# Optimization experiments

Hardware: AMD Instinct MI355X
Metric: run time of the kernel (lower is better)

## Reference

```python
import jax, jax.numpy as jnp
import numpy as np

N_NODES = 100000
IN_DIM = 128
HIDDEN = 64
N_EDGES = 1600000


def setup_inputs() -> dict:
    key = jax.random.key(0)
    k_z, k_e, k_w1, k_b1, k_w2, k_b2 = jax.random.split(key, 6)
    z = jax.random.normal(k_z, (N_NODES, IN_DIM), dtype=jnp.float32)
    edge_index = jax.random.randint(k_e, (2, N_EDGES), 0, N_NODES, dtype=jnp.int64)
    # PyTorch Linear stores weight [out, in]; keep [in, out] layout for x @ W
    bound1 = 1.0 / np.sqrt(2 * IN_DIM)
    W1 = jax.random.uniform(k_w1, (2 * IN_DIM, HIDDEN), jnp.float32, -bound1, bound1)
    b1 = jax.random.uniform(k_b1, (HIDDEN,), jnp.float32, -bound1, bound1)
    bound2 = 1.0 / np.sqrt(HIDDEN)
    W2 = jax.random.uniform(k_w2, (HIDDEN, 1), jnp.float32, -bound2, bound2)
    b2 = jax.random.uniform(k_b2, (1,), jnp.float32, -bound2, bound2)
    return {"z": z, "edge_index": edge_index, "W1": W1, "b1": b1, "W2": W2, "b2": b2}


def reference(z, edge_index, W1, b1, W2, b2):
    src = edge_index[0]
    dst = edge_index[1]
    # gather node features and concat: [E, 2*D]
    edge_feat = jnp.concatenate([z[src], z[dst]], axis=-1)
    h = jax.nn.relu(edge_feat @ W1 + b1)  # [E, H]
    logits = h @ W2 + b2                  # [E, 1]
    return jax.nn.sigmoid(logits).squeeze(-1)  # [E]
```

## Files before the change

kernel.cpp:

```cpp
#include <hip/hip_runtime.h>
#include <hip/hip_bf16.h>

#define N_NODES 100000
#define IN_DIM  128
#define HIDDEN  64
#define N_EDGES 1600000

typedef unsigned short u16;
typedef unsigned int   u32;
typedef unsigned char  u8;

typedef __attribute__((ext_vector_type(8))) short bf16x8;
typedef __attribute__((ext_vector_type(4))) float f32x4;
typedef __attribute__((ext_vector_type(2))) float f32x2;

__device__ __forceinline__ u16 f2bf(float f) {
    u32 u = __float_as_uint(f);
    u32 r = 0x7FFFu + ((u >> 16) & 1u);
    u += r;
    return (u16)(u >> 16);
}

__device__ __forceinline__ u8 f2fp8(float f) {
    u32 p = (u32)__builtin_amdgcn_cvt_pk_fp8_f32(f, f, 0, false);
    return (u8)(p & 0xFF);
}

__global__ __launch_bounds__(256) void prep_kernel(const float* __restrict__ W1,
                                                   u16* __restrict__ WcatT) {
    int idx = blockIdx.x * 256 + threadIdx.x;
    int jj = idx >> 7;
    int k  = idx & 127;
    float v = (jj < 64) ? W1[k * 64 + jj] : W1[(128 + k) * 64 + (jj - 64)];
    WcatT[idx] = f2bf(v);
}

#define LDK 136
#define GEMM_BLOCKS 625

__global__ __launch_bounds__(256) void gemm_kernel(const float* __restrict__ z,
                                                   const u16* __restrict__ WcatT,
                                                   const float* __restrict__ b1,
                                                   u8* __restrict__ UVq) {
    __shared__ u16 Bs[128 * LDK];

    int tid = threadIdx.x;
    for (int c = tid; c < 128 * 16; c += 256) {
        int row = c >> 4, cc = c & 15;
        *(uint4*)(Bs + row * LDK + cc * 8) = *(const uint4*)(WcatT + row * 128 + cc * 8);
    }
    __syncthreads();

    int wave = tid >> 6;
    int lane = tid & 63;
    int quad = lane >> 4;
    int l16  = lane & 15;

    int gwid   = blockIdx.x * 4 + wave;
    int nwaves = GEMM_BLOCKS * 4;
    const int NTILES = N_NODES / 16;

    float bias[4];
#pragma unroll
    for (int nt = 0; nt < 4; nt++) bias[nt] = b1[nt * 16 + l16];

    for (int t = gwid; t < NTILES; t += nwaves) {
        const float* zrow = z + (size_t)(t * 16 + l16) * 128;

        float4 fa[8];
#pragma unroll
        for (int kb = 0; kb < 4; kb++) {
            fa[kb * 2]     = *(const float4*)(zrow + kb * 32 + quad * 8);
            fa[kb * 2 + 1] = *(const float4*)(zrow + kb * 32 + quad * 8 + 4);
        }
        bf16x8 afrag[4];
#pragma unroll
        for (int kb = 0; kb < 4; kb++) {
            union { bf16x8 v; u32 w[4]; } pk;
            float4 lo = fa[kb * 2], hi = fa[kb * 2 + 1];
            pk.w[0] = (u32)f2bf(lo.x) | ((u32)f2bf(lo.y) << 16);
            pk.w[1] = (u32)f2bf(lo.z) | ((u32)f2bf(lo.w) << 16);
            pk.w[2] = (u32)f2bf(hi.x) | ((u32)f2bf(hi.y) << 16);
            pk.w[3] = (u32)f2bf(hi.z) | ((u32)f2bf(hi.w) << 16);
            afrag[kb] = pk.v;
        }

        f32x4 acc[8];
        const f32x4 z4 = {0.f, 0.f, 0.f, 0.f};
#pragma unroll
        for (int i = 0; i < 8; i++) acc[i] = z4;

#pragma unroll
        for (int kb = 0; kb < 4; kb++) {
            int k0 = kb * 32 + quad * 8;
#pragma unroll
            for (int nt = 0; nt < 8; nt++) {
                bf16x8 b = *(const bf16x8*)(Bs + (nt * 16 + l16) * LDK + k0);
                acc[nt] = __builtin_amdgcn_mfma_f32_16x16x32_bf16(afrag[kb], b, acc[nt], 0, 0, 0);
            }
        }

#pragma unroll
        for (int nt = 0; nt < 8; nt++) {
            float bb = (nt < 4) ? bias[nt] : 0.f;
#pragma unroll
            for (int r = 0; r < 4; r++) {
                int row = t * 16 + quad * 4 + r;
                UVq[(size_t)row * 128 + nt * 16 + l16] = f2fp8(acc[nt][r] + bb);
            }
        }
    }
}

#define BATCH 8

__global__ __launch_bounds__(256, 2) void edge_kernel(const int* __restrict__ ei,
                                                      const u8* __restrict__ UVq,
                                                      const float* __restrict__ W2,
                                                      const float* __restrict__ b2,
                                                      float* __restrict__ out) {
    int gwave = (blockIdx.x * 256 + threadIdx.x) >> 6;
    int lane  = threadIdx.x & 63;
    int sub   = lane >> 3;
    int c     = lane & 7;

    float4 w2a = *(const float4*)(W2 + c * 8);
    float4 w2b = *(const float4*)(W2 + c * 8 + 4);
    float w2r[8] = {w2a.x, w2a.y, w2a.z, w2a.w, w2b.x, w2b.y, w2b.z, w2b.w};
    float b2v = b2[0];

    int ebase = gwave * 64 + sub;

    int sB[BATCH], dB[BATCH];
#pragma unroll
    for (int j = 0; j < BATCH; j++) {
        int e = ebase + j * 8;
        sB[j] = __builtin_nontemporal_load(ei + e);
        dB[j] = __builtin_nontemporal_load(ei + N_EDGES + e);
    }
    uint2 aB[BATCH], bB[BATCH];
#pragma unroll
    for (int j = 0; j < BATCH; j++) {
        aB[j] = *(const uint2*)(UVq + (size_t)sB[j] * 128 + c * 8);
        bB[j] = *(const uint2*)(UVq + (size_t)dB[j] * 128 + 64 + c * 8);
    }
    __builtin_amdgcn_sched_barrier(0);

#pragma unroll
    for (int j = 0; j < BATCH; j++) {
        u32 aw[2] = {aB[j].x, aB[j].y};
        u32 bw[2] = {bB[j].x, bB[j].y};
        float acc = 0.f;
#pragma unroll
        for (int i = 0; i < 2; i++) {
            f32x2 uu0 = __builtin_amdgcn_cvt_pk_f32_fp8(aw[i], false);
            f32x2 vv0 = __builtin_amdgcn_cvt_pk_f32_fp8(bw[i], false);
            f32x2 uu1 = __builtin_amdgcn_cvt_pk_f32_fp8(aw[i], true);
            f32x2 vv1 = __builtin_amdgcn_cvt_pk_f32_fp8(bw[i], true);
            float h0 = fmaxf(uu0.x + vv0.x, 0.f);
            float h1 = fmaxf(uu0.y + vv0.y, 0.f);
            float h2 = fmaxf(uu1.x + vv1.x, 0.f);
            float h3 = fmaxf(uu1.y + vv1.y, 0.f);
            acc = fmaf(h0, w2r[i * 4 + 0], acc);
            acc = fmaf(h1, w2r[i * 4 + 1], acc);
            acc = fmaf(h2, w2r[i * 4 + 2], acc);
            acc = fmaf(h3, w2r[i * 4 + 3], acc);
        }
        acc += __shfl_xor(acc, 1);
        acc += __shfl_xor(acc, 2);
        acc += __shfl_xor(acc, 4);
        if (c == 0) {
            float x = acc + b2v;
            __builtin_nontemporal_store(1.f / (1.f + __expf(-x)), out + ebase + j * 8);
        }
    }
}

extern "C" void kernel_launch(void* const* d_in, const int* in_sizes, int n_in,
                              void* d_out, int out_size, void* d_ws, size_t ws_size,
                              hipStream_t stream) {
    const float* z  = (const float*)d_in[0];
    const int*   ei = (const int*)d_in[1];
    const float* W1 = (const float*)d_in[2];
    const float* b1 = (const float*)d_in[3];
    const float* W2 = (const float*)d_in[4];
    const float* b2 = (const float*)d_in[5];
    float* out = (float*)d_out;

    u16* WcatT = (u16*)d_ws;
    u8*  UVq   = (u8*)((char*)d_ws + 65536);

    prep_kernel<<<64, 256, 0, stream>>>(W1, WcatT);
    gemm_kernel<<<GEMM_BLOCKS, 256, 0, stream>>>(z, WcatT, b1, UVq);
    edge_kernel<<<6250, 256, 0, stream>>>(ei, UVq, W2, b2, out);
}
```

Before: 151.6 us.

## Fuse weight prep into GEMM and use 4 lanes per edge with 16B gathers

Removes the separate weight-prep kernel by having each GEMM block transpose and convert W1 to bf16 directly into shared memory, saving a launch. The edge kernel now assigns 4 lanes per edge with 16-byte fp8 gathers instead of 8 lanes with 8-byte gathers, cutting shuffle steps and load instructions. It drops the explicit batched load prefetch and occupancy hint, which may reduce memory-level parallelism, and the redundant per-block W1 conversion adds work.

```diff
diff --git a/kernel.cpp b/kernel.cpp
--- a/kernel.cpp
+++ b/kernel.cpp
@@ -26,28 +26,21 @@
     return (u8)(p & 0xFF);
 }
 
-__global__ __launch_bounds__(256) void prep_kernel(const float* __restrict__ W1,
-                                                   u16* __restrict__ WcatT) {
-    int idx = blockIdx.x * 256 + threadIdx.x;
-    int jj = idx >> 7;
-    int k  = idx & 127;
-    float v = (jj < 64) ? W1[k * 64 + jj] : W1[(128 + k) * 64 + (jj - 64)];
-    WcatT[idx] = f2bf(v);
-}
-
 #define LDK 136
 #define GEMM_BLOCKS 625
 
 __global__ __launch_bounds__(256) void gemm_kernel(const float* __restrict__ z,
-                                                   const u16* __restrict__ WcatT,
+                                                   const float* __restrict__ W1,
                                                    const float* __restrict__ b1,
                                                    u8* __restrict__ UVq) {
     __shared__ u16 Bs[128 * LDK];
 
     int tid = threadIdx.x;
-    for (int c = tid; c < 128 * 16; c += 256) {
-        int row = c >> 4, cc = c & 15;
-        *(uint4*)(Bs + row * LDK + cc * 8) = *(const uint4*)(WcatT + row * 128 + cc * 8);
+    for (int cIdx = tid; cIdx < 8192; cIdx += 256) {
+        int k  = cIdx >> 6;
+        int jj = cIdx & 63;
+        Bs[jj * LDK + k]        = f2bf(W1[k * 64 + jj]);
+        Bs[(64 + jj) * LDK + k] = f2bf(W1[(128 + k) * 64 + jj]);
     }
     __syncthreads();
 
@@ -112,66 +105,53 @@
     }
 }
 
-#define BATCH 8
-
-__global__ __launch_bounds__(256, 2) void edge_kernel(const int* __restrict__ ei,
-                                                      const u8* __restrict__ UVq,
-                                                      const float* __restrict__ W2,
-                                                      const float* __restrict__ b2,
-                                                      float* __restrict__ out) {
+__global__ __launch_bounds__(256) void edge_kernel(const int* __restrict__ ei,
+                                                   const u8* __restrict__ UVq,
+                                                   const float* __restrict__ W2,
+                                                   const float* __restrict__ b2,
+                                                   float* __restrict__ out) {
     int gwave = (blockIdx.x * 256 + threadIdx.x) >> 6;
     int lane  = threadIdx.x & 63;
-    int sub   = lane >> 3;
-    int c     = lane & 7;
+    int sub   = lane >> 2;
+    int c     = lane & 3;
 
-    float4 w2a = *(const float4*)(W2 + c * 8);
-    float4 w2b = *(const float4*)(W2 + c * 8 + 4);
-    float w2r[8] = {w2a.x, w2a.y, w2a.z, w2a.w, w2b.x, w2b.y, w2b.z, w2b.w};
+    float w2r[16];
+#pragma unroll
+    for (int i = 0; i < 4; i++) {
+        float4 t = *(const float4*)(W2 + c * 16 + i * 4);
+        w2r[i * 4 + 0] = t.x; w2r[i * 4 + 1] = t.y;
+        w2r[i * 4 + 2] = t.z; w2r[i * 4 + 3] = t.w;
+    }
     float b2v = b2[0];
 
     int ebase = gwave * 64 + sub;
 
-    int sB[BATCH], dB[BATCH];
 #pragma unroll
-    for (int j = 0; j < BATCH; j++) {
-        int e = ebase + j * 8;
-        sB[j] = __builtin_nontemporal_load(ei + e);
-        dB[j] = __builtin_nontemporal_load(ei + N_EDGES + e);
-    }
-    uint2 aB[BATCH], bB[BATCH];
-#pragma unroll
-    for (int j = 0; j < BATCH; j++) {
-        aB[j] = *(const uint2*)(UVq + (size_t)sB[j] * 128 + c * 8);
-        bB[j] = *(const uint2*)(UVq + (size_t)dB[j] * 128 + 64 + c * 8);
-    }
-    __builtin_amdgcn_sched_barrier(0);
-
-#pragma unroll
-    for (int j = 0; j < BATCH; j++) {
-        u32 aw[2] = {aB[j].x, aB[j].y};
-        u32 bw[2] = {bB[j].x, bB[j].y};
+    for (int it = 0; it < 4; ++it) {
+        int e = ebase + it * 16;
+        int s = __builtin_nontemporal_load(ei + e);
+        int d = __builtin_nontemporal_load(ei + N_EDGES + e);
+        uint4 a = *(const uint4*)(UVq + (size_t)s * 128 + c * 16);
+        uint4 b = *(const uint4*)(UVq + (size_t)d * 128 + 64 + c * 16);
+        u32 aw[4] = {a.x, a.y, a.z, a.w};
+        u32 bw[4] = {b.x, b.y, b.z, b.w};
         float acc = 0.f;
 #pragma unroll
-        for (int i = 0; i < 2; i++) {
+        for (int i = 0; i < 4; i++) {
             f32x2 uu0 = __builtin_amdgcn_cvt_pk_f32_fp8(aw[i], false);
             f32x2 vv0 = __builtin_amdgcn_cvt_pk_f32_fp8(bw[i], false);
             f32x2 uu1 = __builtin_amdgcn_cvt_pk_f32_fp8(aw[i], true);
             f32x2 vv1 = __builtin_amdgcn_cvt_pk_f32_fp8(bw[i], true);
-            float h0 = fmaxf(uu0.x + vv0.x, 0.f);
-            float h1 = fmaxf(uu0.y + vv0.y, 0.f);
-            float h2 = fmaxf(uu1.x + vv1.x, 0.f);
-            float h3 = fmaxf(uu1.y + vv1.y, 0.f);
-            acc = fmaf(h0, w2r[i * 4 + 0], acc);
-            acc = fmaf(h1, w2r[i * 4 + 1], acc);
-            acc = fmaf(h2, w2r[i * 4 + 2], acc);
-            acc = fmaf(h3, w2r[i * 4 + 3], acc);
+            acc = fmaf(fmaxf(uu0.x + vv0.x, 0.f), w2r[i * 4 + 0], acc);
+            acc = fmaf(fmaxf(uu0.y + vv0.y, 0.f), w2r[i * 4 + 1], acc);
+            acc = fmaf(fmaxf(uu1.x + vv1.x, 0.f), w2r[i * 4 + 2], acc);
+            acc = fmaf(fmaxf(uu1.y + vv1.y, 0.f), w2r[i * 4 + 3], acc);
         }
         acc += __shfl_xor(acc, 1);
         acc += __shfl_xor(acc, 2);
-        acc += __shfl_xor(acc, 4);
         if (c == 0) {
             float x = acc + b2v;
-            __builtin_nontemporal_store(1.f / (1.f + __expf(-x)), out + ebase + j * 8);
+            __builtin_nontemporal_store(1.f / (1.f + __expf(-x)), out + e);
         }
     }
 }
@@ -187,10 +167,8 @@
     const float* b2 = (const float*)d_in[5];
     float* out = (float*)d_out;
 
-    u16* WcatT = (u16*)d_ws;
-    u8*  UVq   = (u8*)((char*)d_ws + 65536);
+    u8* UVq = (u8*)d_ws;
 
-    prep_kernel<<<64, 256, 0, stream>>>(W1, WcatT);
-    gemm_kernel<<<GEMM_BLOCKS, 256, 0, stream>>>(z, WcatT, b1, UVq);
+    gemm_kernel<<<GEMM_BLOCKS, 256, 0, stream>>>(z, W1, b1, UVq);
     edge_kernel<<<6250, 256, 0, stream>>>(ei, UVq, W2, b2, out);
 }
```

Result: slower. 155.5 us (+2.5%).
